# Kernel tuning notes

Measured on AMD Instinct MI355X. Metric: run time of the kernel, lower is better.

The kernel has to match this reference:

```python
import jax, jax.numpy as jnp
import numpy as np

B, NQ, NK = 16, 4096, 77
QUERY_DIM, CONTEXT_DIM = 512, 768
HEADS, D_HEAD = 8, 64
INNER = HEADS * D_HEAD  # 512
SCALE = D_HEAD ** -0.5


def setup_inputs() -> dict:
    key = jax.random.key(0)
    ks = jax.random.split(key, 7)
    x = jax.random.normal(ks[0], (B, NQ, QUERY_DIM), dtype=jnp.float32)
    context = jax.random.normal(ks[1], (B, NK, CONTEXT_DIM), dtype=jnp.float32)
    # Linear weights stored as [in, out] (x @ W), matching nn.Linear math W^T.
    Wq = jax.random.normal(ks[2], (QUERY_DIM, INNER), dtype=jnp.float32) / np.sqrt(QUERY_DIM)
    Wk = jax.random.normal(ks[3], (CONTEXT_DIM, INNER), dtype=jnp.float32) / np.sqrt(CONTEXT_DIM)
    Wv = jax.random.normal(ks[4], (CONTEXT_DIM, INNER), dtype=jnp.float32) / np.sqrt(CONTEXT_DIM)
    Wo = jax.random.normal(ks[5], (INNER, QUERY_DIM), dtype=jnp.float32) / np.sqrt(INNER)
    bo = jax.random.normal(ks[6], (QUERY_DIM,), dtype=jnp.float32) * 0.02
    return {"x": x, "context": context, "Wq": Wq, "Wk": Wk, "Wv": Wv, "Wo": Wo, "bo": bo}


def reference(x, context, Wq, Wk, Wv, Wo, bo):
    b, nq, _ = x.shape
    nk = context.shape[1]
    # projections (no bias for q/k/v, as in the module)
    q = (x @ Wq).reshape(b, nq, HEADS, D_HEAD).transpose(0, 2, 1, 3)       # b h nq d
    k = (context @ Wk).reshape(b, nk, HEADS, D_HEAD).transpose(0, 2, 1, 3)  # b h nk d
    v = (context @ Wv).reshape(b, nk, HEADS, D_HEAD).transpose(0, 2, 1, 3)  # b h nk d
    # softmax(QK^T * scale) V  -- same math as the chunked torch loop
    sim = jnp.einsum('bhid,bhjd->bhij', q, k) * SCALE                       # b h nq nk
    attn = jax.nn.softmax(sim, axis=-1)
    out = jnp.einsum('bhij,bhjd->bhid', attn, v)                            # b h nq d
    out = out.transpose(0, 2, 1, 3).reshape(b, nq, INNER)                   # b nq (h d)
    return out @ Wo + bo
```

## Files before the change

### kernel.cpp

```cpp
#include <hip/hip_runtime.h>
#include <hip/hip_bf16.h>
#include <stdint.h>


typedef __attribute__((ext_vector_type(8))) short bf16x8;
typedef __attribute__((ext_vector_type(4))) float f32x4;
typedef __attribute__((ext_vector_type(4))) short short4v;
typedef __attribute__((ext_vector_type(4))) float float4v;
typedef __attribute__((ext_vector_type(2))) unsigned uint2v;
typedef __attribute__((ext_vector_type(4))) unsigned uint4v;

#define DEVINL __device__ __forceinline__

DEVINL short f2bf(float f) {
  unsigned u = __builtin_bit_cast(unsigned, f);
  unsigned r = (u + 0x7FFFu + ((u >> 16) & 1u)) >> 16;
  return (short)(unsigned short)r;
}

DEVINL unsigned pkbf(float lo, float hi) {
  unsigned r;
  asm("v_cvt_pk_bf16_f32 %0, %1, %2" : "=v"(r) : "v"(lo), "v"(hi));
  return r;
}

#define GLDS16(gp, sp)                                                \
  __builtin_amdgcn_global_load_lds(                                   \
      (const __attribute__((address_space(1))) void*)(gp),            \
      (__attribute__((address_space(3))) void*)(sp), 16, 0, 0)

__global__ __launch_bounds__(256) void prep_all(
    const float* __restrict__ Wq, const float* __restrict__ Wk,
    const float* __restrict__ Wv, const float* __restrict__ Wo,
    short* __restrict__ wqt, short* __restrict__ wkt,
    short* __restrict__ wvt, short* __restrict__ wot,
    float4v* __restrict__ vfill) {
  const int z = blockIdx.z;
  if (z == 4) {
    for (int i = (blockIdx.y * 8 + blockIdx.x) * 256 + threadIdx.x;
         i < 106496; i += 24576)
      vfill[i] = float4v{0.f, 0.f, 0.f, 0.f};
    return;
  }
  const float* W;
  short* Wt;
  int K;
  switch (z) {
    case 0: W = Wq; Wt = wqt; K = 512; break;
    case 1: W = Wk; Wt = wkt; K = 768; break;
    case 2: W = Wv; Wt = wvt; K = 768; break;
    default: W = Wo; Wt = wot; K = 512; break;
  }
  const int kt = blockIdx.y * 64;
  if (kt >= K) return;
  const int nt = blockIdx.x * 64;

  __shared__ short Tl[64][65];
#pragma unroll
  for (int i = 0; i < 16; ++i) {
    int idx = threadIdx.x + i * 256;
    int r = idx >> 6, c = idx & 63;
    Tl[c][r] = f2bf(W[(size_t)(kt + r) * 512 + nt + c]);
  }
  __syncthreads();
#pragma unroll
  for (int i = 0; i < 16; ++i) {
    int idx = threadIdx.x + i * 256;
    int r = idx >> 6, c = idx & 63;
    Wt[(size_t)(nt + r) * K + kt + c] = Tl[r][c];
  }
}

__global__ __launch_bounds__(256) void kvproj(const float* __restrict__ A,
                                              const short* __restrict__ wkt,
                                              const short* __restrict__ wvt,
                                              short* __restrict__ Kb,
                                              short* __restrict__ Vtg) {
  __shared__ short Al[32][40];
  __shared__ short Bl[128][40];

  const int TRANS = blockIdx.z;
  const short* Bt = TRANS ? wvt : wkt;

  const int tid = threadIdx.x;
  const int lane = tid & 63, wid = tid >> 6;
  const int wm = wid >> 1, wn = wid & 1;
  const int quad = lane >> 4, l16 = lane & 15;
  const int m0 = blockIdx.y * 32, n0 = blockIdx.x * 128;
  const int M = 1232, K = 768;

  f32x4 acc[4] = {};

  for (int k0 = 0; k0 < K; k0 += 32) {
    for (int idx = tid; idx < 32 * 8; idx += 256) {
      int row = idx >> 3, kq = idx & 7;
      float4v v = {};
      if (m0 + row < M)
        v = *(const float4v*)(A + (size_t)(m0 + row) * K + k0 + kq * 4);
      short4v s = {f2bf(v[0]), f2bf(v[1]), f2bf(v[2]), f2bf(v[3])};
      *(short4v*)&Al[row][kq * 4] = s;
    }
    for (int idx = tid; idx < 512; idx += 256) {
      int row = idx >> 2, kq = idx & 3;
      *(bf16x8*)&Bl[row][kq * 8] =
          *(const bf16x8*)(Bt + (size_t)(n0 + row) * K + k0 + kq * 8);
    }
    __syncthreads();

    bf16x8 a = *(bf16x8*)&Al[wm * 16 + l16][quad * 8];
#pragma unroll
    for (int n = 0; n < 4; ++n) {
      bf16x8 b = *(bf16x8*)&Bl[wn * 64 + n * 16 + l16][quad * 8];
      acc[n] = __builtin_amdgcn_mfma_f32_16x16x32_bf16(a, b, acc[n], 0, 0, 0);
    }
    __syncthreads();
  }

#pragma unroll
  for (int n = 0; n < 4; ++n) {
    const int col = n0 + wn * 64 + n * 16 + l16;
    const int rowb = m0 + wm * 16 + quad * 4;
#pragma unroll
    for (int r = 0; r < 4; ++r) {
      const int rr = rowb + r;
      if (rr < M) {
        if (!TRANS) {
          Kb[(size_t)rr * 512 + col] = f2bf(acc[n][r]);
        } else {
          const int bb = rr / 77, key = rr - bb * 77;
          Vtg[(size_t)((bb * 8 + (col >> 6)) * 64 + (col & 63)) * 104 + key] =
              f2bf(acc[n][r]);
        }
      }
    }
  }
}

__global__ __launch_bounds__(512, 4) void qattn(const float* __restrict__ x,
                                                const short* __restrict__ wqt,
                                                const short* __restrict__ Kb,
                                                const short* __restrict__ Vtg,
                                                short* __restrict__ AOb) {
  __shared__ __align__(16) char smem[63744];
  short* xb  = (short*)smem;
  short* wsW = (short*)(smem + 20480);
  short* Qh  = (short*)smem;
  short* Kl  = (short*)(smem + 18432);
  short* Vt  = (short*)(smem + 29952);
  short* Pw  = (short*)(smem + 43264);

  const int tid = threadIdx.x;
  const int lane = tid & 63, w = tid >> 6;
  const int wm = w >> 2, wn = w & 3;
  const int quad = lane >> 4, l16 = lane & 15;
  const int qt = blockIdx.x & 511, ch = blockIdx.x >> 9;
  const int m0 = qt * 128;
  const int b = qt >> 5;
  const int n0 = ch * 256;

  f32x4 acc[4][4] = {};

  const int xrow = tid >> 2, xcol = (tid & 3) * 8;
  const int wlr = lane >> 2, wlc = (lane & 3) * 8;

  const float* xg = x + (size_t)(m0 + xrow) * 512 + xcol;

  float4v pxa, pxb;
  pxa = *(const float4v*)(xg);
  pxb = *(const float4v*)(xg + 4);
#pragma unroll
  for (int p = 0; p < 2; ++p) {
    const int rowb = (w * 2 + p) * 16;
    GLDS16(wqt + (size_t)(n0 + rowb + wlr) * 512 + wlc, wsW + rowb * 32);
  }

  for (int t = 0; t < 16; ++t) {
    short* xbuf = xb + (t & 1) * 5120;
    short* wbuf = wsW + (t & 1) * 8192;

    uint4v u = {pkbf(pxa[0], pxa[1]), pkbf(pxa[2], pxa[3]),
                pkbf(pxb[0], pxb[1]), pkbf(pxb[2], pxb[3])};
    *(bf16x8*)&xbuf[xrow * 40 + xcol] = __builtin_bit_cast(bf16x8, u);

    __syncthreads();

    if (t < 15) {
      const int k1 = (t + 1) * 32;
#pragma unroll
      for (int p = 0; p < 2; ++p) {
        const int rowb = (w * 2 + p) * 16;
        GLDS16(wqt + (size_t)(n0 + rowb + wlr) * 512 + k1 + wlc,
               wsW + ((t + 1) & 1) * 8192 + rowb * 32);
      }
      pxa = *(const float4v*)(xg + k1);
      pxb = *(const float4v*)(xg + k1 + 4);
    }

    bf16x8 af[4], bfr[4];
#pragma unroll
    for (int m = 0; m < 4; ++m)
      af[m] = *(bf16x8*)&xbuf[(wm * 64 + m * 16 + l16) * 40 + quad * 8];
#pragma unroll
    for (int n = 0; n < 4; ++n)
      bfr[n] = *(bf16x8*)&wbuf[(wn * 64 + n * 16 + l16) * 32 + quad * 8];
    __builtin_amdgcn_s_setprio(1);
#pragma unroll
    for (int m = 0; m < 4; ++m)
#pragma unroll
      for (int n = 0; n < 4; ++n)
        acc[m][n] = __builtin_amdgcn_mfma_f32_16x16x32_bf16(af[m], bfr[n],
                                                            acc[m][n], 0, 0, 0);
    __builtin_amdgcn_s_setprio(0);
  }
  __syncthreads();

#pragma unroll
  for (int it = 0; it < 4; ++it) {
    if (it) __syncthreads();
    const int h = ch * 4 + it;

    if (wn == it) {
#pragma unroll
      for (int m = 0; m < 4; ++m)
#pragma unroll
        for (int n = 0; n < 4; ++n)
#pragma unroll
          for (int r = 0; r < 4; ++r)
            Qh[(wm * 64 + m * 16 + quad * 4 + r) * 72 + n * 16 + l16] =
                f2bf(acc[m][n][r]);
    }
    for (int idx = tid; idx < 616; idx += 512) {
      const int r = idx >> 3, cc = (idx & 7) * 8;
      *(bf16x8*)&Kl[r * 72 + cc] =
          *(const bf16x8*)(Kb + ((size_t)b * 77 + r) * 512 + h * 64 + cc);
    }
    for (int cid = w; cid < 13; cid += 8)
      GLDS16(Vtg + (size_t)(b * 8 + h) * 6656 + cid * 512 + lane * 8,
             Vt + cid * 512);
    __syncthreads();

    bf16x8 qfr[2];
#pragma unroll
    for (int ks = 0; ks < 2; ++ks)
      qfr[ks] = *(bf16x8*)&Qh[(w * 16 + l16) * 72 + ks * 32 + quad * 8];

    f32x4 c[5] = {};
    __builtin_amdgcn_s_setprio(1);
#pragma unroll
    for (int f = 0; f < 5; ++f)
#pragma unroll
      for (int ks = 0; ks < 2; ++ks) {
        bf16x8 a = *(bf16x8*)&Kl[(f * 16 + l16) * 72 + ks * 32 + quad * 8];
        c[f] = __builtin_amdgcn_mfma_f32_16x16x32_bf16(a, qfr[ks], c[f], 0, 0, 0);
      }
    __builtin_amdgcn_s_setprio(0);

    float mx = -1e30f;
#pragma unroll
    for (int f = 0; f < 5; ++f)
#pragma unroll
      for (int r = 0; r < 4; ++r) {
        const int key = f * 16 + quad * 4 + r;
        float v = c[f][r] * 0.125f;
        v = (key < 77) ? v : -1e30f;
        c[f][r] = v;
        mx = fmaxf(mx, v);
      }
    mx = fmaxf(mx, __shfl_xor(mx, 16));
    mx = fmaxf(mx, __shfl_xor(mx, 32));

    short* pbase = Pw + (w * 16 + l16) * 80;
    float sum = 0.f;
#pragma unroll
    for (int f = 0; f < 5; ++f) {
      float e0 = __expf(c[f][0] - mx), e1 = __expf(c[f][1] - mx);
      float e2 = __expf(c[f][2] - mx), e3 = __expf(c[f][3] - mx);
      sum += (e0 + e1) + (e2 + e3);
      uint2v sv2 = {pkbf(e0, e1), pkbf(e2, e3)};
      *(uint2v*)(pbase + f * 16 + quad * 4) = sv2;
    }
    sum += __shfl_xor(sum, 16);
    sum += __shfl_xor(sum, 32);
    const float inv = 1.0f / sum;

    bf16x8 pb0 = *(bf16x8*)(pbase + quad * 8);
    bf16x8 pb1 = *(bf16x8*)(pbase + 32 + quad * 8);
    bf16x8 pb2 = bf16x8{0, 0, 0, 0, 0, 0, 0, 0};
    if (quad < 2) pb2 = *(bf16x8*)(pbase + 64 + quad * 8);

    f32x4 o[4] = {};
    __builtin_amdgcn_s_setprio(1);
#pragma unroll
    for (int mt = 0; mt < 4; ++mt) {
      const short* vrow = &Vt[(mt * 16 + l16) * 104];
      o[mt] = __builtin_amdgcn_mfma_f32_16x16x32_bf16(
          *(bf16x8*)(vrow + quad * 8), pb0, o[mt], 0, 0, 0);
      o[mt] = __builtin_amdgcn_mfma_f32_16x16x32_bf16(
          *(bf16x8*)(vrow + 32 + quad * 8), pb1, o[mt], 0, 0, 0);
      o[mt] = __builtin_amdgcn_mfma_f32_16x16x32_bf16(
          *(bf16x8*)(vrow + 64 + quad * 8), pb2, o[mt], 0, 0, 0);
    }
    __builtin_amdgcn_s_setprio(0);

    short* op = AOb + ((size_t)m0 + w * 16 + l16) * 512 + h * 64;
#pragma unroll
    for (int mt = 0; mt < 4; ++mt) {
      uint2v sv2 = {pkbf(o[mt][0] * inv, o[mt][1] * inv),
                    pkbf(o[mt][2] * inv, o[mt][3] * inv)};
      *(uint2v*)(op + mt * 16 + quad * 4) = sv2;
    }
  }
}

__global__ __launch_bounds__(256) void gemm2(const short* __restrict__ A,
                                             const short* __restrict__ Bt,
                                             float* __restrict__ C,
                                             const float* __restrict__ bias) {
  __shared__ short As[2][128 * 32];
  __shared__ short Bs[2][128 * 32];

  const int tid = threadIdx.x;
  const int lane = tid & 63, w = tid >> 6;
  const int wm = w >> 1, wn = w & 1;
  const int quad = lane >> 4, l16 = lane & 15;

  const int cpx = gridDim.x >> 3;
  const int swz = (blockIdx.x & 7) * cpx + (blockIdx.x >> 3);
  const int m0 = (swz >> 2) * 128, n0 = (swz & 3) * 128;

  const int lr = lane >> 2, lc = (lane & 3) * 8;

  f32x4 acc[4][4] = {};

#pragma unroll
  for (int p = 0; p < 2; ++p) {
    const int rowb = (w * 2 + p) * 16;
    GLDS16(A + (size_t)(m0 + rowb + lr) * 512 + lc, &As[0][rowb * 32]);
    GLDS16(Bt + (size_t)(n0 + rowb + lr) * 512 + lc, &Bs[0][rowb * 32]);
  }
  __syncthreads();

  for (int t = 0; t < 16; ++t) {
    const int cur = t & 1;
    if (t < 15) {
      const int k1 = (t + 1) * 32;
#pragma unroll
      for (int p = 0; p < 2; ++p) {
        const int rowb = (w * 2 + p) * 16;
        GLDS16(A + (size_t)(m0 + rowb + lr) * 512 + k1 + lc,
               &As[cur ^ 1][rowb * 32]);
        GLDS16(Bt + (size_t)(n0 + rowb + lr) * 512 + k1 + lc,
               &Bs[cur ^ 1][rowb * 32]);
      }
    }
    bf16x8 af[4], bfr[4];
#pragma unroll
    for (int m = 0; m < 4; ++m)
      af[m] = *(bf16x8*)&As[cur][(wm * 64 + m * 16 + l16) * 32 + quad * 8];
#pragma unroll
    for (int n = 0; n < 4; ++n)
      bfr[n] = *(bf16x8*)&Bs[cur][(wn * 64 + n * 16 + l16) * 32 + quad * 8];
#pragma unroll
    for (int m = 0; m < 4; ++m)
#pragma unroll
      for (int n = 0; n < 4; ++n)
        acc[m][n] = __builtin_amdgcn_mfma_f32_16x16x32_bf16(af[m], bfr[n],
                                                            acc[m][n], 0, 0, 0);
    if (t < 15) __syncthreads();
  }

#pragma unroll
  for (int m = 0; m < 4; ++m)
#pragma unroll
    for (int n = 0; n < 4; ++n) {
      const int col = n0 + wn * 64 + n * 16 + l16;
      const int rowb = m0 + wm * 64 + m * 16 + quad * 4;
      const float badd = bias[col];
#pragma unroll
      for (int r = 0; r < 4; ++r)
        C[(size_t)(rowb + r) * 512 + col] = acc[m][n][r] + badd;
    }
}

extern "C" void kernel_launch(void* const* d_in, const int* in_sizes, int n_in,
                              void* d_out, int out_size, void* d_ws, size_t ws_size,
                              hipStream_t stream) {
  const float* x   = (const float*)d_in[0];
  const float* ctx = (const float*)d_in[1];
  const float* Wq  = (const float*)d_in[2];
  const float* Wk  = (const float*)d_in[3];
  const float* Wv  = (const float*)d_in[4];
  const float* Wo  = (const float*)d_in[5];
  const float* bo  = (const float*)d_in[6];
  float* out = (float*)d_out;

  char* ws = (char*)d_ws;
  size_t off = 0;
  short* wqt = (short*)(ws + off); off += 512 * 512 * 2;
  short* wkt = (short*)(ws + off); off += 768 * 512 * 2;
  short* wvt = (short*)(ws + off); off += 768 * 512 * 2;
  short* wot = (short*)(ws + off); off += 512 * 512 * 2;
  short* Kb  = (short*)(ws + off); off += 1232 * 512 * 2;
  short* Vtg = (short*)(ws + off); off += (size_t)16 * 8 * 64 * 104 * 2;
  short* AOb = (short*)(ws + off); off += (size_t)65536 * 512 * 2;

  prep_all<<<dim3(8, 12, 5), 256, 0, stream>>>(Wq, Wk, Wv, Wo,
                                               wqt, wkt, wvt, wot,
                                               (float4v*)Vtg);
  kvproj<<<dim3(4, 39, 2), 256, 0, stream>>>(ctx, wkt, wvt, Kb, Vtg);

  qattn<<<1024, 512, 0, stream>>>(x, wqt, Kb, Vtg, AOb);

  gemm2<<<2048, 256, 0, stream>>>(AOb, wot, out, bo);
}
```

Measured before the change: 178.5 us.

## Process each wave's head slice independently, reading K/V directly from global

Each wave now converts its own Q accumulator tiles to bf16 and runs attention for the head matching its column group, using a private LDS slice. This replaces the four block-wide iterations and their syncthreads barriers. K and V^T are no longer staged in LDS; MFMA operands are loaded straight from global memory, relying on cache reuse, and the LDS footprint shrinks accordingly. The trade-off is global-load latency inside the MFMA loops and possible reads past the 77 valid key rows (rows up to 79), which are masked but may fall outside the buffer for the last batch.

```diff
diff --git a/kernel.cpp b/kernel.cpp
--- a/kernel.cpp
+++ b/kernel.cpp
@@ -141,13 +141,11 @@
                                                 const short* __restrict__ Kb,
                                                 const short* __restrict__ Vtg,
                                                 short* __restrict__ AOb) {
-  __shared__ __align__(16) char smem[63744];
+  __shared__ __align__(16) char smem[53248];
   short* xb  = (short*)smem;
   short* wsW = (short*)(smem + 20480);
-  short* Qh  = (short*)smem;
-  short* Kl  = (short*)(smem + 18432);
-  short* Vt  = (short*)(smem + 29952);
-  short* Pw  = (short*)(smem + 43264);
+  short* Qsl = (short*)smem;
+  short* Pw  = (short*)(smem + 18432);
 
   const int tid = threadIdx.x;
   const int lane = tid & 63, w = tid >> 6;
@@ -214,44 +212,33 @@
   }
   __syncthreads();
 
-#pragma unroll
-  for (int it = 0; it < 4; ++it) {
-    if (it) __syncthreads();
-    const int h = ch * 4 + it;
-
-    if (wn == it) {
-#pragma unroll
-      for (int m = 0; m < 4; ++m)
-#pragma unroll
-        for (int n = 0; n < 4; ++n)
-#pragma unroll
-          for (int r = 0; r < 4; ++r)
-            Qh[(wm * 64 + m * 16 + quad * 4 + r) * 72 + n * 16 + l16] =
-                f2bf(acc[m][n][r]);
-    }
-    for (int idx = tid; idx < 616; idx += 512) {
-      const int r = idx >> 3, cc = (idx & 7) * 8;
-      *(bf16x8*)&Kl[r * 72 + cc] =
-          *(const bf16x8*)(Kb + ((size_t)b * 77 + r) * 512 + h * 64 + cc);
-    }
-    for (int cid = w; cid < 13; cid += 8)
-      GLDS16(Vtg + (size_t)(b * 8 + h) * 6656 + cid * 512 + lane * 8,
-             Vt + cid * 512);
-    __syncthreads();
+  const int h = ch * 4 + wn;
+  short* qsl = Qsl + w * 1152;
+  short* psl = Pw + w * 1280;
+  const short* kg = Kb + (size_t)b * 77 * 512 + h * 64;
+  const short* vg = Vtg + (size_t)(b * 8 + h) * 6656;
+
+#pragma unroll
+  for (int c = 0; c < 4; ++c) {
+#pragma unroll
+    for (int n = 0; n < 4; ++n)
+#pragma unroll
+      for (int r = 0; r < 4; ++r)
+        qsl[(quad * 4 + r) * 72 + n * 16 + l16] = f2bf(acc[c][n][r]);
 
     bf16x8 qfr[2];
-#pragma unroll
-    for (int ks = 0; ks < 2; ++ks)
-      qfr[ks] = *(bf16x8*)&Qh[(w * 16 + l16) * 72 + ks * 32 + quad * 8];
-
-    f32x4 c[5] = {};
+    qfr[0] = *(bf16x8*)&qsl[l16 * 72 + quad * 8];
+    qfr[1] = *(bf16x8*)&qsl[l16 * 72 + 32 + quad * 8];
+
+    f32x4 cc[5] = {};
     __builtin_amdgcn_s_setprio(1);
 #pragma unroll
     for (int f = 0; f < 5; ++f)
 #pragma unroll
       for (int ks = 0; ks < 2; ++ks) {
-        bf16x8 a = *(bf16x8*)&Kl[(f * 16 + l16) * 72 + ks * 32 + quad * 8];
-        c[f] = __builtin_amdgcn_mfma_f32_16x16x32_bf16(a, qfr[ks], c[f], 0, 0, 0);
+        bf16x8 a = *(const bf16x8*)(kg + (size_t)(f * 16 + l16) * 512 +
+                                    ks * 32 + quad * 8);
+        cc[f] = __builtin_amdgcn_mfma_f32_16x16x32_bf16(a, qfr[ks], cc[f], 0, 0, 0);
       }
     __builtin_amdgcn_s_setprio(0);
 
@@ -261,20 +248,20 @@
 #pragma unroll
       for (int r = 0; r < 4; ++r) {
         const int key = f * 16 + quad * 4 + r;
-        float v = c[f][r] * 0.125f;
+        float v = cc[f][r] * 0.125f;
         v = (key < 77) ? v : -1e30f;
-        c[f][r] = v;
+        cc[f][r] = v;
         mx = fmaxf(mx, v);
       }
     mx = fmaxf(mx, __shfl_xor(mx, 16));
     mx = fmaxf(mx, __shfl_xor(mx, 32));
 
-    short* pbase = Pw + (w * 16 + l16) * 80;
+    short* pbase = psl + l16 * 80;
     float sum = 0.f;
 #pragma unroll
     for (int f = 0; f < 5; ++f) {
-      float e0 = __expf(c[f][0] - mx), e1 = __expf(c[f][1] - mx);
-      float e2 = __expf(c[f][2] - mx), e3 = __expf(c[f][3] - mx);
+      float e0 = __expf(cc[f][0] - mx), e1 = __expf(cc[f][1] - mx);
+      float e2 = __expf(cc[f][2] - mx), e3 = __expf(cc[f][3] - mx);
       sum += (e0 + e1) + (e2 + e3);
       uint2v sv2 = {pkbf(e0, e1), pkbf(e2, e3)};
       *(uint2v*)(pbase + f * 16 + quad * 4) = sv2;
@@ -292,17 +279,17 @@
     __builtin_amdgcn_s_setprio(1);
 #pragma unroll
     for (int mt = 0; mt < 4; ++mt) {
-      const short* vrow = &Vt[(mt * 16 + l16) * 104];
+      const short* vrow = vg + (size_t)(mt * 16 + l16) * 104;
       o[mt] = __builtin_amdgcn_mfma_f32_16x16x32_bf16(
-          *(bf16x8*)(vrow + quad * 8), pb0, o[mt], 0, 0, 0);
+          *(const bf16x8*)(vrow + quad * 8), pb0, o[mt], 0, 0, 0);
       o[mt] = __builtin_amdgcn_mfma_f32_16x16x32_bf16(
-          *(bf16x8*)(vrow + 32 + quad * 8), pb1, o[mt], 0, 0, 0);
+          *(const bf16x8*)(vrow + 32 + quad * 8), pb1, o[mt], 0, 0, 0);
       o[mt] = __builtin_amdgcn_mfma_f32_16x16x32_bf16(
-          *(bf16x8*)(vrow + 64 + quad * 8), pb2, o[mt], 0, 0, 0);
+          *(const bf16x8*)(vrow + 64 + quad * 8), pb2, o[mt], 0, 0, 0);
     }
     __builtin_amdgcn_s_setprio(0);
 
-    short* op = AOb + ((size_t)m0 + w * 16 + l16) * 512 + h * 64;
+    short* op = AOb + ((size_t)m0 + wm * 64 + c * 16 + l16) * 512 + h * 64;
 #pragma unroll
     for (int mt = 0; mt < 4; ++mt) {
       uint2v sv2 = {pkbf(o[mt][0] * inv, o[mt][1] * inv),
```

New measurement: 209.9 us. 1.18x slower.
